# Kernel optimization log

Measured on AMD Instinct MI355X. Metric: run time of the kernel, lower is better.

The kernel has to match this reference:

```python
import jax, jax.numpy as jnp
import numpy as np

NUM_HEADS = 16

def setup_inputs() -> dict:
    key = jax.random.key(0)
    ks = jax.random.split(key, 6)
    B, N, E = 2, 2048, 2048
    QK, V, M = 2048, 2048, 4096
    x = jax.random.normal(ks[0], (B, N, E), dtype=jnp.float32)
    Wq = jax.random.normal(ks[1], (QK, E), dtype=jnp.float32) * 0.02
    k_weight = jax.random.normal(ks[2], (M, QK), dtype=jnp.float32) * 0.05
    v_weight = jax.random.normal(ks[3], (M, V), dtype=jnp.float32) * 0.05
    Wg = jax.random.normal(ks[4], (V, E), dtype=jnp.float32) * 0.02
    Wout = jax.random.normal(ks[5], (E, V), dtype=jnp.float32) * 0.02
    return {"x": x, "Wq": Wq, "k_weight": k_weight, "v_weight": v_weight, "Wg": Wg, "Wout": Wout}

def reference(x, Wq, k_weight, v_weight, Wg, Wout):
    H = NUM_HEADS
    B, N, E = x.shape
    M = k_weight.shape[0]
    # q: [B, N, QK] -> [B, H, N, dk]
    q = jnp.einsum('bne,fe->bnf', x, Wq)
    dk = q.shape[-1] // H
    q = q.reshape(B, N, H, dk).transpose(0, 2, 1, 3)
    # k: [M, QK] -> [H, M, dk]; v: [M, V] -> [H, M, dv]
    k = k_weight.reshape(M, H, dk).transpose(1, 0, 2)
    dv = v_weight.shape[1] // H
    v = v_weight.reshape(M, H, dv).transpose(1, 0, 2)
    scale = jnp.asarray(dk, x.dtype) ** 0.5  # use_scale == 1
    k = k * scale
    v = v * scale
    # non-softmax attention over fixed memory
    energy = jax.nn.silu(jnp.einsum('bhnd,hmd->bhnm', q, k))  # [B,H,N,M]
    out = jnp.einsum('bhnm,hmd->bhnd', energy, v)  # [B,H,N,dv]
    out = out.transpose(0, 2, 1, 3).reshape(B, N, H * dv)
    # output gate (silu)
    gate = jax.nn.silu(jnp.einsum('bne,ve->bnv', x, Wg))
    out = out * gate
    return jnp.einsum('bnv,ev->bne', out, Wout)
```

## Files before the change

### kernel.cpp

```cpp
#include <hip/hip_runtime.h>

typedef __bf16 bf16;
typedef __bf16 bf16x4 __attribute__((ext_vector_type(4)));
typedef __bf16 bf16x8 __attribute__((ext_vector_type(8)));
typedef float f32x4 __attribute__((ext_vector_type(4)));

#define MFMA(a, b, c) __builtin_amdgcn_mfma_f32_16x16x32_bf16(a, b, c, 0, 0, 0)

__device__ __forceinline__ void gload_lds16(const void* g, void* l) {
  __builtin_amdgcn_global_load_lds(
      (const __attribute__((address_space(1))) void*)g,
      (__attribute__((address_space(3))) void*)l, 16, 0, 0);
}

__global__ __launch_bounds__(256) void cvt_bf16(const float* __restrict__ in,
                                                bf16* __restrict__ out, int n) {
  int i = (blockIdx.x * 256 + threadIdx.x) * 4;
  if (i >= n) return;
  float4 v = *(const float4*)(in + i);
  bf16x4 o = {(bf16)v.x, (bf16)v.y, (bf16)v.z, (bf16)v.w};
  *(bf16x4*)(out + i) = o;
}

__global__ __launch_bounds__(256) void transpose_v_cvt(const float* __restrict__ v,
                                                       bf16* __restrict__ vt) {
  __shared__ bf16 T[64 * 72];
  const int m0 = blockIdx.x * 64, c0 = blockIdx.y * 64;
  const int tid = threadIdx.x;
  const int tr = tid >> 3;
  const int tc = (tid & 7) << 3;
#pragma unroll
  for (int it = 0; it < 2; it++) {
    int r = tr + it * 32;
    const float* src = v + (long)(m0 + r) * 2048 + c0 + tc;
    float4 a = *(const float4*)src;
    float4 b = *(const float4*)(src + 4);
    bf16x8 t = {(bf16)a.x, (bf16)a.y, (bf16)a.z, (bf16)a.w,
                (bf16)b.x, (bf16)b.y, (bf16)b.z, (bf16)b.w};
    *(bf16x8*)&T[r * 72 + tc] = t;
  }
  __syncthreads();
#pragma unroll
  for (int it = 0; it < 2; it++) {
    int c = tr + it * 32;
    bf16x8 o;
#pragma unroll
    for (int j = 0; j < 8; j++) o[j] = T[(tc + j) * 72 + c];
    *(bf16x8*)(vt + (long)(c0 + c) * 4096 + m0 + tc) = o;
  }
}

template <int MODE>
__global__ __launch_bounds__(256, 2) void gemm_bt(const bf16* __restrict__ A,
                                                  const bf16* __restrict__ B,
                                                  const bf16* __restrict__ other,
                                                  bf16* __restrict__ Cb,
                                                  float* __restrict__ Cf, int M, int N, int K) {
  __shared__ bf16 As[128 * 32];
  __shared__ bf16 Bs[128 * 32];
  const int tid = threadIdx.x;
  const int wave = tid >> 6, lane = tid & 63;
  const int wr = wave >> 1, wc = wave & 1;
  const long bM = (long)blockIdx.y * 128, bN = (long)blockIdx.x * 128;

  f32x4 acc[4][4] = {};

  const int srow = (wave << 5) + (lane >> 2);
  const int sg = ((lane & 3) ^ ((lane >> 3) & 3)) << 3;
  const bf16* Ag = A + (bM + srow) * (long)K + sg;
  const bf16* Bg = B + (bN + srow) * (long)K + sg;
  bf16* Asl = &As[srow * 32 + ((lane & 3) << 3)];
  bf16* Bsl = &Bs[srow * 32 + ((lane & 3) << 3)];

  const int fr = lane & 15;
  const int gofs = (((lane >> 4) ^ ((fr >> 1) & 3)) << 3);

  for (int k0 = 0; k0 < K; k0 += 32) {
    __syncthreads();
    gload_lds16(Ag + k0, Asl);
    gload_lds16(Ag + k0 + (long)16 * K, Asl + 16 * 32);
    gload_lds16(Bg + k0, Bsl);
    gload_lds16(Bg + k0 + (long)16 * K, Bsl + 16 * 32);
    __syncthreads();
    bf16x8 af[4], bfv[4];
#pragma unroll
    for (int i = 0; i < 4; i++)
      af[i] = *(const bf16x8*)&As[(wr * 64 + i * 16 + fr) * 32 + gofs];
#pragma unroll
    for (int j = 0; j < 4; j++)
      bfv[j] = *(const bf16x8*)&Bs[(wc * 64 + j * 16 + fr) * 32 + gofs];
#pragma unroll
    for (int i = 0; i < 4; i++)
#pragma unroll
      for (int j = 0; j < 4; j++) acc[i][j] = MFMA(af[i], bfv[j], acc[i][j]);
  }

  const int er = wr * 64 + ((lane >> 4) << 2);
  const int ec = wc * 64 + (lane & 15);
#pragma unroll
  for (int i = 0; i < 4; i++)
#pragma unroll
    for (int j = 0; j < 4; j++)
#pragma unroll
      for (int r = 0; r < 4; r++) {
        long row = bM + er + i * 16 + r;
        long col = bN + ec + j * 16;
        float v = acc[i][j][r];
        if (MODE == 1) {
          float g = v / (1.f + __expf(-v));
          v = g * (float)other[row * (long)N + col];
        }
        if (MODE == 2)
          Cf[row * (long)N + col] = v;
        else
          Cb[row * (long)N + col] = (bf16)v;
      }
}

__global__ __launch_bounds__(256, 2) void attn_fused(const bf16* __restrict__ q,
                                                     const bf16* __restrict__ kw,
                                                     const bf16* __restrict__ vt,
                                                     bf16* __restrict__ attn) {
  constexpr int E = 2048, M = 4096, NQ = 2048;
  constexpr float scale = 11.3137085f;
  const int bid = blockIdx.x;
  const int h = ((bid & 7) << 1) | ((bid >> 8) & 1);
  const int sub = (bid >> 3) & 31;
  const int b = sub >> 4, nt = sub & 15;

  const int tid = threadIdx.x, wave = tid >> 6, lane = tid & 63;
  const int wr = wave >> 1, wc = wave & 1;
  const int fr = lane & 15, fk = (lane >> 4) << 3;
  const int quad = lane >> 4;

  __shared__ bf16 Ks[64 * 128];
  __shared__ bf16 Vts[128 * 64];
  __shared__ bf16 Ps[128 * 64];

  const bf16* qbase = q + (long)(b * NQ + nt * 128) * E + h * 128;
  bf16x8 qf[4][4];
#pragma unroll
  for (int i = 0; i < 4; i++)
#pragma unroll
    for (int ks = 0; ks < 4; ks++)
      qf[i][ks] = *(const bf16x8*)(qbase + (long)(wr * 64 + i * 16 + fr) * E + ks * 32 + fk);

  f32x4 oacc[4][4] = {};

  const int krow = (wave << 4) + quad;
  bf16* ksl = &Ks[krow * 128 + ((lane & 15) << 3)];
  const bf16* kg = kw + (long)krow * E + h * 128;

  const int vrow = (wave << 5) + (lane >> 3);
  const int vg_ofs = ((lane & 7) ^ ((lane >> 3) & 7)) << 3;
  const bf16* vg = vt + (long)(h * 128 + vrow) * M + vg_ofs;
  bf16* vsl = &Vts[vrow * 64 + ((lane & 7) << 3)];

  for (int m0 = 0; m0 < M; m0 += 64) {
    __syncthreads();
#pragma unroll
    for (int i = 0; i < 4; i++) {
      int kswz = ((lane & 15) ^ ((quad + 4 * i) & 15)) << 3;
      gload_lds16(kg + (long)(m0 + i * 4) * E + kswz, ksl + i * 4 * 128);
      gload_lds16(vg + m0 + (long)i * 8 * M, vsl + i * 8 * 64);
    }
    __syncthreads();

    f32x4 sacc[4][2] = {};
#pragma unroll
    for (int ks = 0; ks < 4; ks++) {
      bf16x8 kf[2];
#pragma unroll
      for (int jm = 0; jm < 2; jm++)
        kf[jm] = *(const bf16x8*)&Ks[(wc * 32 + jm * 16 + fr) * 128 +
                                     (((ks * 4 + quad) ^ fr) << 3)];
#pragma unroll
      for (int i = 0; i < 4; i++)
#pragma unroll
        for (int jm = 0; jm < 2; jm++) sacc[i][jm] = MFMA(qf[i][ks], kf[jm], sacc[i][jm]);
    }
#pragma unroll
    for (int i = 0; i < 4; i++)
#pragma unroll
      for (int jm = 0; jm < 2; jm++)
#pragma unroll
        for (int r = 0; r < 4; r++) {
          float s = sacc[i][jm][r] * scale;
          float e = s / (1.f + __expf(-s));
          int n = wr * 64 + i * 16 + quad * 4 + r;
          int m = wc * 32 + jm * 16 + (lane & 15);
          Ps[n * 64 + (((m >> 3) ^ (n & 7)) << 3) + (m & 7)] = (bf16)e;
        }
    __syncthreads();

#pragma unroll
    for (int ks = 0; ks < 2; ks++) {
      const int pvo = (((ks * 4 + quad) ^ (fr & 7)) << 3);
      bf16x8 pf[4], vf[4];
#pragma unroll
      for (int i = 0; i < 4; i++)
        pf[i] = *(const bf16x8*)&Ps[(wr * 64 + i * 16 + fr) * 64 + pvo];
#pragma unroll
      for (int j = 0; j < 4; j++)
        vf[j] = *(const bf16x8*)&Vts[(wc * 64 + j * 16 + fr) * 64 + pvo];
#pragma unroll
      for (int i = 0; i < 4; i++)
#pragma unroll
        for (int j = 0; j < 4; j++) oacc[i][j] = MFMA(pf[i], vf[j], oacc[i][j]);
    }
  }

  bf16* obase = attn + (long)(b * NQ + nt * 128) * E + h * 128;
#pragma unroll
  for (int i = 0; i < 4; i++)
#pragma unroll
    for (int j = 0; j < 4; j++)
#pragma unroll
      for (int r = 0; r < 4; r++) {
        int n = wr * 64 + i * 16 + quad * 4 + r;
        int dv = wc * 64 + j * 16 + (lane & 15);
        obase[(long)n * E + dv] = (bf16)(oacc[i][j][r] * scale);
      }
}

extern "C" void kernel_launch(void* const* d_in, const int* in_sizes, int n_in,
                              void* d_out, int out_size, void* d_ws, size_t ws_size,
                              hipStream_t stream) {
  const float* x = (const float*)d_in[0];
  const float* Wq = (const float*)d_in[1];
  const float* kw = (const float*)d_in[2];
  const float* vw = (const float*)d_in[3];
  const float* Wg = (const float*)d_in[4];
  const float* Wout = (const float*)d_in[5];
  float* out = (float*)d_out;
  bf16* ws = (bf16*)d_ws;

  bf16* xb = ws;
  bf16* Wqb = ws + 8388608;
  bf16* kwb = ws + 12582912;
  bf16* vt = ws + 20971520;
  bf16* q = ws + 29360128;
  bf16* attn = ws + 37748736;

  cvt_bf16<<<8192, 256, 0, stream>>>(x, xb, 8388608);
  cvt_bf16<<<4096, 256, 0, stream>>>(Wq, Wqb, 4194304);
  cvt_bf16<<<8192, 256, 0, stream>>>(kw, kwb, 8388608);
  transpose_v_cvt<<<dim3(64, 32), 256, 0, stream>>>(vw, vt);
  gemm_bt<0><<<dim3(16, 32), 256, 0, stream>>>(xb, Wqb, (const bf16*)nullptr, q, (float*)nullptr,
                                               4096, 2048, 2048);
  attn_fused<<<512, 256, 0, stream>>>(q, kwb, vt, attn);
  cvt_bf16<<<4096, 256, 0, stream>>>(Wg, Wqb, 4194304);
  gemm_bt<1><<<dim3(16, 32), 256, 0, stream>>>(xb, Wqb, attn, q, (float*)nullptr, 4096, 2048,
                                               2048);
  cvt_bf16<<<4096, 256, 0, stream>>>(Wout, kwb, 4194304);
  gemm_bt<2><<<dim3(16, 32), 256, 0, stream>>>(q, kwb, (const bf16*)nullptr, (bf16*)nullptr, out,
                                               4096, 2048, 2048);
}
```

Baseline: 541.8 us.

## Fuse Q and gate GEMMs, halve attention tile, fold gate multiply into attention

The Q projection and the gate projection now share one launch with a doubled grid. The gate half applies SiLU in its epilogue and the Q half pre-multiplies by the scale. The attention kernel uses 64-row query tiles with a 4-blocks-per-CU launch bound and 1024 blocks, computes K·Q^T with a fast exp2/rcp SiLU and vectorized P stores, then multiplies the gate in place in its epilogue. This removes one GEMM launch and a separate gate-multiply pass, and aims for better occupancy in attention. In exchange, each block loads K/V tiles for only 64 query rows, so K/V traffic per query roughly doubles, and register pressure must fit the tighter launch bound.

```diff
diff --git a/kernel.cpp b/kernel.cpp
--- a/kernel.cpp
+++ b/kernel.cpp
@@ -6,6 +6,11 @@
 typedef float f32x4 __attribute__((ext_vector_type(4)));
 
 #define MFMA(a, b, c) __builtin_amdgcn_mfma_f32_16x16x32_bf16(a, b, c, 0, 0, 0)
+
+__device__ __forceinline__ float fast_silu(float x) {
+  float e = __builtin_amdgcn_exp2f(x * -1.4426950408889634f);
+  return x * __builtin_amdgcn_rcpf(1.f + e);
+}
 
 __device__ __forceinline__ void gload_lds16(const void* g, void* l) {
   __builtin_amdgcn_global_load_lds(
@@ -53,22 +58,26 @@
 template <int MODE>
 __global__ __launch_bounds__(256, 2) void gemm_bt(const bf16* __restrict__ A,
                                                   const bf16* __restrict__ B,
-                                                  const bf16* __restrict__ other,
-                                                  bf16* __restrict__ Cb,
+                                                  const bf16* __restrict__ B2,
+                                                  bf16* __restrict__ C1,
+                                                  bf16* __restrict__ C2,
                                                   float* __restrict__ Cf, int M, int N, int K) {
   __shared__ bf16 As[128 * 32];
   __shared__ bf16 Bs[128 * 32];
   const int tid = threadIdx.x;
   const int wave = tid >> 6, lane = tid & 63;
   const int wr = wave >> 1, wc = wave & 1;
-  const long bM = (long)blockIdx.y * 128, bN = (long)blockIdx.x * 128;
+  const bool gsel = (MODE == 3) && (blockIdx.x >= 16);
+  const bf16* Bm = gsel ? B2 : B;
+  const long bM = (long)blockIdx.y * 128;
+  const long bN = (long)((MODE == 3) ? (blockIdx.x & 15) : blockIdx.x) * 128;
 
   f32x4 acc[4][4] = {};
 
   const int srow = (wave << 5) + (lane >> 2);
   const int sg = ((lane & 3) ^ ((lane >> 3) & 3)) << 3;
   const bf16* Ag = A + (bM + srow) * (long)K + sg;
-  const bf16* Bg = B + (bN + srow) * (long)K + sg;
+  const bf16* Bg = Bm + (bN + srow) * (long)K + sg;
   bf16* Asl = &As[srow * 32 + ((lane & 3) << 3)];
   bf16* Bsl = &Bs[srow * 32 + ((lane & 3) << 3)];
 
@@ -106,120 +115,130 @@
         long row = bM + er + i * 16 + r;
         long col = bN + ec + j * 16;
         float v = acc[i][j][r];
-        if (MODE == 1) {
-          float g = v / (1.f + __expf(-v));
-          v = g * (float)other[row * (long)N + col];
+        if (MODE == 2) {
+          Cf[row * (long)N + col] = v;
+        } else {
+          if (gsel)
+            C2[row * (long)N + col] = (bf16)fast_silu(v);
+          else
+            C1[row * (long)N + col] = (bf16)(v * 11.3137085f);
         }
-        if (MODE == 2)
-          Cf[row * (long)N + col] = v;
-        else
-          Cb[row * (long)N + col] = (bf16)v;
       }
 }
 
-__global__ __launch_bounds__(256, 2) void attn_fused(const bf16* __restrict__ q,
+__global__ __launch_bounds__(256, 4) void attn_fused(const bf16* __restrict__ q,
                                                      const bf16* __restrict__ kw,
                                                      const bf16* __restrict__ vt,
-                                                     bf16* __restrict__ attn) {
-  constexpr int E = 2048, M = 4096, NQ = 2048;
+                                                     bf16* __restrict__ gate_io) {
+  constexpr int E = 2048, M = 4096;
   constexpr float scale = 11.3137085f;
   const int bid = blockIdx.x;
-  const int h = ((bid & 7) << 1) | ((bid >> 8) & 1);
-  const int sub = (bid >> 3) & 31;
-  const int b = sub >> 4, nt = sub & 15;
+  const int h = ((bid & 7) << 1) | ((bid >> 9) & 1);
+  const int b = (bid >> 8) & 1;
+  const int nt = (bid >> 3) & 31;
+  const long n0 = (long)b * 2048 + nt * 64;
 
   const int tid = threadIdx.x, wave = tid >> 6, lane = tid & 63;
-  const int wr = wave >> 1, wc = wave & 1;
-  const int fr = lane & 15, fk = (lane >> 4) << 3;
-  const int quad = lane >> 4;
+  const int quad = lane >> 4, ln = lane & 15;
+  const int sw_m = wave & 1, sw_n = wave >> 1;
+  const int pw_n = wave & 1, pw_dv = wave >> 1;
 
   __shared__ bf16 Ks[64 * 128];
   __shared__ bf16 Vts[128 * 64];
-  __shared__ bf16 Ps[128 * 64];
-
-  const bf16* qbase = q + (long)(b * NQ + nt * 128) * E + h * 128;
-  bf16x8 qf[4][4];
-#pragma unroll
-  for (int i = 0; i < 4; i++)
+  __shared__ bf16 Ps[64 * 64];
+
+  const bf16* qbase = q + (n0 + sw_n * 32) * E + h * 128;
+  bf16x8 qf[2][4];
+#pragma unroll
+  for (int t = 0; t < 2; t++)
 #pragma unroll
     for (int ks = 0; ks < 4; ks++)
-      qf[i][ks] = *(const bf16x8*)(qbase + (long)(wr * 64 + i * 16 + fr) * E + ks * 32 + fk);
-
-  f32x4 oacc[4][4] = {};
-
-  const int krow = (wave << 4) + quad;
-  bf16* ksl = &Ks[krow * 128 + ((lane & 15) << 3)];
-  const bf16* kg = kw + (long)krow * E + h * 128;
-
-  const int vrow = (wave << 5) + (lane >> 3);
-  const int vg_ofs = ((lane & 7) ^ ((lane >> 3) & 7)) << 3;
-  const bf16* vg = vt + (long)(h * 128 + vrow) * M + vg_ofs;
-  bf16* vsl = &Vts[vrow * 64 + ((lane & 7) << 3)];
+      qf[t][ks] = *(const bf16x8*)(qbase + (long)(t * 16 + ln) * E + ks * 32 + (quad << 3));
+
+  f32x4 oacc[2][4] = {};
+
+  const bf16* kg = kw + (long)((wave << 4) + quad) * E + h * 128;
+  bf16* ksl = &Ks[(wave << 4) * 128 + lane * 8];
+  int kc[4];
+#pragma unroll
+  for (int i = 0; i < 4; i++) kc[i] = (ln ^ ((quad + i * 4) & 15)) << 3;
+
+  const bf16* vg = vt + (long)(h * 128 + (wave << 5) + (lane >> 3)) * M +
+                   (((lane & 7) ^ ((lane >> 3) & 7)) << 3);
+  bf16* vsl = &Vts[(wave << 5) * 64 + lane * 8];
+
+  int waddr[2][2];
+#pragma unroll
+  for (int mt = 0; mt < 2; mt++)
+#pragma unroll
+    for (int n2 = 0; n2 < 2; n2++) {
+      int n = sw_n * 32 + n2 * 16 + ln;
+      int mb8 = sw_m * 4 + mt * 2 + (quad >> 1);
+      waddr[mt][n2] = n * 64 + ((mb8 ^ (n & 7)) << 3) + ((quad & 1) << 2);
+    }
 
   for (int m0 = 0; m0 < M; m0 += 64) {
     __syncthreads();
 #pragma unroll
     for (int i = 0; i < 4; i++) {
-      int kswz = ((lane & 15) ^ ((quad + 4 * i) & 15)) << 3;
-      gload_lds16(kg + (long)(m0 + i * 4) * E + kswz, ksl + i * 4 * 128);
+      gload_lds16(kg + (long)(m0 + i * 4) * E + kc[i], ksl + i * 4 * 128);
       gload_lds16(vg + m0 + (long)i * 8 * M, vsl + i * 8 * 64);
     }
     __syncthreads();
 
-    f32x4 sacc[4][2] = {};
+    f32x4 sacc[2][2] = {};
 #pragma unroll
     for (int ks = 0; ks < 4; ks++) {
-      bf16x8 kf[2];
-#pragma unroll
-      for (int jm = 0; jm < 2; jm++)
-        kf[jm] = *(const bf16x8*)&Ks[(wc * 32 + jm * 16 + fr) * 128 +
-                                     (((ks * 4 + quad) ^ fr) << 3)];
-#pragma unroll
-      for (int i = 0; i < 4; i++)
-#pragma unroll
-        for (int jm = 0; jm < 2; jm++) sacc[i][jm] = MFMA(qf[i][ks], kf[jm], sacc[i][jm]);
-    }
-#pragma unroll
-    for (int i = 0; i < 4; i++)
-#pragma unroll
-      for (int jm = 0; jm < 2; jm++)
-#pragma unroll
-        for (int r = 0; r < 4; r++) {
-          float s = sacc[i][jm][r] * scale;
-          float e = s / (1.f + __expf(-s));
-          int n = wr * 64 + i * 16 + quad * 4 + r;
-          int m = wc * 32 + jm * 16 + (lane & 15);
-          Ps[n * 64 + (((m >> 3) ^ (n & 7)) << 3) + (m & 7)] = (bf16)e;
-        }
+      bf16x8 af[2];
+#pragma unroll
+      for (int mt = 0; mt < 2; mt++)
+        af[mt] = *(const bf16x8*)&Ks[(sw_m * 32 + mt * 16 + ln) * 128 +
+                                     (((ks * 4 + quad) ^ ln) << 3)];
+#pragma unroll
+      for (int mt = 0; mt < 2; mt++)
+#pragma unroll
+        for (int n2 = 0; n2 < 2; n2++) sacc[mt][n2] = MFMA(af[mt], qf[n2][ks], sacc[mt][n2]);
+    }
+
+#pragma unroll
+    for (int mt = 0; mt < 2; mt++)
+#pragma unroll
+      for (int n2 = 0; n2 < 2; n2++) {
+        bf16x4 p;
+#pragma unroll
+        for (int r = 0; r < 4; r++) p[r] = (bf16)fast_silu(sacc[mt][n2][r]);
+        *(bf16x4*)&Ps[waddr[mt][n2]] = p;
+      }
     __syncthreads();
 
 #pragma unroll
     for (int ks = 0; ks < 2; ks++) {
-      const int pvo = (((ks * 4 + quad) ^ (fr & 7)) << 3);
-      bf16x8 pf[4], vf[4];
-#pragma unroll
-      for (int i = 0; i < 4; i++)
-        pf[i] = *(const bf16x8*)&Ps[(wr * 64 + i * 16 + fr) * 64 + pvo];
-#pragma unroll
-      for (int j = 0; j < 4; j++)
-        vf[j] = *(const bf16x8*)&Vts[(wc * 64 + j * 16 + fr) * 64 + pvo];
-#pragma unroll
-      for (int i = 0; i < 4; i++)
-#pragma unroll
-        for (int j = 0; j < 4; j++) oacc[i][j] = MFMA(pf[i], vf[j], oacc[i][j]);
-    }
-  }
-
-  bf16* obase = attn + (long)(b * NQ + nt * 128) * E + h * 128;
-#pragma unroll
-  for (int i = 0; i < 4; i++)
-#pragma unroll
-    for (int j = 0; j < 4; j++)
+      const int so = ((ks * 4 + quad) ^ (ln & 7)) << 3;
+      bf16x8 pf[2], vf[4];
+#pragma unroll
+      for (int n2 = 0; n2 < 2; n2++)
+        pf[n2] = *(const bf16x8*)&Ps[(pw_n * 32 + n2 * 16 + ln) * 64 + so];
+#pragma unroll
+      for (int dt = 0; dt < 4; dt++)
+        vf[dt] = *(const bf16x8*)&Vts[(pw_dv * 64 + dt * 16 + ln) * 64 + so];
+#pragma unroll
+      for (int n2 = 0; n2 < 2; n2++)
+#pragma unroll
+        for (int dt = 0; dt < 4; dt++) oacc[n2][dt] = MFMA(pf[n2], vf[dt], oacc[n2][dt]);
+    }
+  }
+
+  bf16* gio = gate_io + n0 * E + h * 128;
+#pragma unroll
+  for (int n2 = 0; n2 < 2; n2++)
+#pragma unroll
+    for (int dt = 0; dt < 4; dt++)
 #pragma unroll
       for (int r = 0; r < 4; r++) {
-        int n = wr * 64 + i * 16 + quad * 4 + r;
-        int dv = wc * 64 + j * 16 + (lane & 15);
-        obase[(long)n * E + dv] = (bf16)(oacc[i][j][r] * scale);
+        int n = pw_n * 32 + n2 * 16 + quad * 4 + r;
+        int dv = pw_dv * 64 + dt * 16 + ln;
+        float g = (float)gio[(long)n * E + dv];
+        gio[(long)n * E + dv] = (bf16)(g * oacc[n2][dt][r] * scale);
       }
 }
 
@@ -235,24 +254,22 @@
   float* out = (float*)d_out;
   bf16* ws = (bf16*)d_ws;
 
-  bf16* xb = ws;
-  bf16* Wqb = ws + 8388608;
-  bf16* kwb = ws + 12582912;
-  bf16* vt = ws + 20971520;
-  bf16* q = ws + 29360128;
-  bf16* attn = ws + 37748736;
-
-  cvt_bf16<<<8192, 256, 0, stream>>>(x, xb, 8388608);
-  cvt_bf16<<<4096, 256, 0, stream>>>(Wq, Wqb, 4194304);
-  cvt_bf16<<<8192, 256, 0, stream>>>(kw, kwb, 8388608);
-  transpose_v_cvt<<<dim3(64, 32), 256, 0, stream>>>(vw, vt);
-  gemm_bt<0><<<dim3(16, 32), 256, 0, stream>>>(xb, Wqb, (const bf16*)nullptr, q, (float*)nullptr,
-                                               4096, 2048, 2048);
-  attn_fused<<<512, 256, 0, stream>>>(q, kwb, vt, attn);
-  cvt_bf16<<<4096, 256, 0, stream>>>(Wg, Wqb, 4194304);
-  gemm_bt<1><<<dim3(16, 32), 256, 0, stream>>>(xb, Wqb, attn, q, (float*)nullptr, 4096, 2048,
+  bf16* S0 = ws;
+  bf16* S1 = ws + 8388608;
+  bf16* S2 = ws + 16777216;
+  bf16* S3 = ws + 25165824;
+  bf16* S4 = ws + 33554432;
+  bf16* Wgb = S1 + 4194304;
+
+  cvt_bf16<<<8192, 256, 0, stream>>>(x, S0, 8388608);
+  cvt_bf16<<<4096, 256, 0, stream>>>(Wq, S1, 4194304);
+  cvt_bf16<<<4096, 256, 0, stream>>>(Wg, Wgb, 4194304);
+  transpose_v_cvt<<<dim3(64, 32), 256, 0, stream>>>(vw, S2);
+  gemm_bt<3><<<dim3(32, 32), 256, 0, stream>>>(S0, S1, Wgb, S3, S4, (float*)nullptr, 4096, 2048,
                                                2048);
-  cvt_bf16<<<4096, 256, 0, stream>>>(Wout, kwb, 4194304);
-  gemm_bt<2><<<dim3(16, 32), 256, 0, stream>>>(q, kwb, (const bf16*)nullptr, (bf16*)nullptr, out,
-                                               4096, 2048, 2048);
-}
+  cvt_bf16<<<8192, 256, 0, stream>>>(kw, S0, 8388608);
+  attn_fused<<<1024, 256, 0, stream>>>(S3, S0, S2, S4);
+  cvt_bf16<<<4096, 256, 0, stream>>>(Wout, S1, 4194304);
+  gemm_bt<2><<<dim3(16, 32), 256, 0, stream>>>(S4, S1, (const bf16*)nullptr, (bf16*)nullptr,
+                                               (bf16*)nullptr, out, 4096, 2048, 2048);
+}
```

Result: faster. 481.4 us (-11.2%).
